# Performance work log

Measured on AMD Instinct MI355X. Metric: run time of the kernel, lower is better.

## Reference

```python
import jax, jax.numpy as jnp
import numpy as np

BLOCK = 64  # bitsandbytes 4-bit blocksize
OUT, IN = 4096, 4096
# NF4 codebook (bitsandbytes values)
NF4_CODE = np.array([
    -1.0, -0.6961928009986877, -0.5250730514526367, -0.39491748809814453,
    -0.28444138169288635, -0.18477343022823334, -0.09105003625154495, 0.0,
    0.07958029955625534, 0.16093020141124725, 0.24611230194568634,
    0.33791524171829224, 0.44070982933044434, 0.5626170039176941,
    0.7229568362236023, 1.0], dtype=np.float32)


def setup_inputs() -> dict:
    key = jax.random.key(0)
    k1, k2, k3 = jax.random.split(key, 3)
    x = jax.random.normal(k1, (8, 2048, IN), dtype=jnp.float32)
    qweight = jax.random.randint(k2, (OUT * IN,), 0, 16, dtype=jnp.int32)
    absmax = jax.random.uniform(k3, (OUT * IN // BLOCK,), dtype=jnp.float32)
    return {"x": x, "qweight": qweight, "absmax": absmax}


def reference(x, qweight, absmax):
    code = jnp.asarray(NF4_CODE)
    # dequantize: codebook lookup, then per-block absmax scaling
    w = code[qweight].reshape(-1, BLOCK) * absmax[:, None]  # [n_blocks, BLOCK]
    W = w.reshape(OUT, IN)                                   # [out, in]
    # linear: y = x @ W^T  (no bias: quantized_bias is None)
    return jnp.einsum('bsi,oi->bso', x, W)
```

## Files before the change

### kernel.cpp

```cpp
#include <hip/hip_runtime.h>
#include <hip/hip_bf16.h>
#include <stdint.h>

#define IN_DIM  4096
#define OUT_DIM 4096
#define M_DIM   16384
#define BK      64
#define NT      (IN_DIM / BK)

typedef float f32x4 __attribute__((ext_vector_type(4)));
typedef short bf16x8 __attribute__((ext_vector_type(8)));
typedef short bf16x4 __attribute__((ext_vector_type(4)));
typedef int   i32x4 __attribute__((ext_vector_type(4)));

__device__ __constant__ float NF4_CODE_D[16] = {
    -1.0f, -0.6961928009986877f, -0.5250730514526367f, -0.39491748809814453f,
    -0.28444138169288635f, -0.18477343022823334f, -0.09105003625154495f, 0.0f,
    0.07958029955625534f, 0.16093020141124725f, 0.24611230194568634f,
    0.33791524171829224f, 0.44070982933044434f, 0.5626170039176941f,
    0.7229568362236023f, 1.0f};

static __device__ __forceinline__ ushort f2bf(float f) {
  union { float f; uint32_t u; } v; v.f = f;
  uint32_t r = v.u + 0x7FFFu + ((v.u >> 16) & 1u);
  return (ushort)(r >> 16);
}

__global__ void dequant_nf4(const int* __restrict__ q, const float* __restrict__ am,
                            ushort* __restrict__ w) {
  __shared__ float code[16];
  if (threadIdx.x < 16) code[threadIdx.x] = NF4_CODE_D[threadIdx.x];
  __syncthreads();
  size_t t = (size_t)blockIdx.x * blockDim.x + threadIdx.x;
  size_t base = t * 8;
  i32x4 qa = *(const i32x4*)(q + base);
  i32x4 qb = *(const i32x4*)(q + base + 4);
  float s = am[base >> 6];
  bf16x8 o;
  o[0] = (short)f2bf(code[qa[0] & 15] * s);
  o[1] = (short)f2bf(code[qa[1] & 15] * s);
  o[2] = (short)f2bf(code[qa[2] & 15] * s);
  o[3] = (short)f2bf(code[qa[3] & 15] * s);
  o[4] = (short)f2bf(code[qb[0] & 15] * s);
  o[5] = (short)f2bf(code[qb[1] & 15] * s);
  o[6] = (short)f2bf(code[qb[2] & 15] * s);
  o[7] = (short)f2bf(code[qb[3] & 15] * s);
  *(bf16x8*)(w + base) = o;
}

__global__ void cvt_x(const float* __restrict__ x, ushort* __restrict__ xb) {
  size_t t = (size_t)blockIdx.x * blockDim.x + threadIdx.x;
  size_t base = t * 8;
  f32x4 a = *(const f32x4*)(x + base);
  f32x4 b = *(const f32x4*)(x + base + 4);
  bf16x8 o;
  o[0] = (short)f2bf(a[0]); o[1] = (short)f2bf(a[1]);
  o[2] = (short)f2bf(a[2]); o[3] = (short)f2bf(a[3]);
  o[4] = (short)f2bf(b[0]); o[5] = (short)f2bf(b[1]);
  o[6] = (short)f2bf(b[2]); o[7] = (short)f2bf(b[3]);
  *(bf16x8*)(xb + base) = o;
}

static __device__ __forceinline__ void llds16(const ushort* g, ushort* l) {
  __builtin_amdgcn_global_load_lds(
      (const __attribute__((address_space(1))) void*)g,
      (__attribute__((address_space(3))) void*)l, 16, 0, 0);
}

__global__ __launch_bounds__(512, 2) void gemm256(const ushort* __restrict__ Xb,
                                                  const ushort* __restrict__ W,
                                                  float* __restrict__ Y) {
  __shared__ ushort As[2][256 * BK];
  __shared__ ushort Bs[2][256 * BK];

  const int tid  = threadIdx.x;
  const int lane = tid & 63;
  const int wid  = tid >> 6;
  const int wr   = wid >> 2;
  const int wc   = wid & 3;
  const int l15  = lane & 15;
  const int kg   = lane >> 4;
  const int l7   = lane & 7;

  const int bid = blockIdx.x;
  const int wg  = (bid & 7) * 128 + (bid >> 3);
  const int tm  = wg >> 4;
  const int tn  = wg & 15;
  const size_t row0 = (size_t)tm * 256;
  const size_t col0 = (size_t)tn * 256;

  const int srow  = tid >> 3;
  const int scol8 = ((tid & 7) ^ (srow & 7)) * 8;
  const int wbase = wid << 9;

  f32x4  acc[8][4] = {};
  bf16x8 aA[4][2], aB[4][2], b0[2][2], b1[2][2];

#define BARX()  __builtin_amdgcn_s_barrier()
#define VMC(n)  asm volatile("s_waitcnt vmcnt(" #n ")" ::: "memory")
#define PRI1()  __builtin_amdgcn_s_setprio(1)
#define PRI0()  __builtin_amdgcn_s_setprio(0)

#define STAGE_A(kt, h, nb) do { \
    llds16(Xb + (row0 + (h)*128 +  0 + srow) * IN_DIM + (kt)*BK + scol8, \
           &As[nb][(h)*8192 +    0 + wbase]); \
    llds16(Xb + (row0 + (h)*128 + 64 + srow) * IN_DIM + (kt)*BK + scol8, \
           &As[nb][(h)*8192 + 4096 + wbase]); \
  } while (0)

#define STAGE_B(kt, h, nb) do { \
    llds16(W + (col0 + (h)*128 +  0 + srow) * IN_DIM + (kt)*BK + scol8, \
           &Bs[nb][(h)*8192 +    0 + wbase]); \
    llds16(W + (col0 + (h)*128 + 64 + srow) * IN_DIM + (kt)*BK + scol8, \
           &Bs[nb][(h)*8192 + 4096 + wbase]); \
  } while (0)

#define LDA_(dst, nb, mh) do { \
    _Pragma("unroll") for (int mi = 0; mi < 4; ++mi) \
    _Pragma("unroll") for (int ks = 0; ks < 2; ++ks) \
      dst[mi][ks] = *(const bf16x8*)&As[nb][((mh)*128 + wr*64 + mi*16 + l15) * BK \
                                            + (((ks*4 + kg) ^ l7) * 8)]; \
  } while (0)

#define LDB_(dst, nb, nh) do { \
    _Pragma("unroll") for (int ni = 0; ni < 2; ++ni) \
    _Pragma("unroll") for (int ks = 0; ks < 2; ++ks) \
      dst[ni][ks] = *(const bf16x8*)&Bs[nb][((nh)*128 + wc*32 + ni*16 + l15) * BK \
                                            + (((ks*4 + kg) ^ l7) * 8)]; \
  } while (0)

#define QUAD(mh, nh, aR, bR) do { PRI1(); \
    _Pragma("unroll") for (int mi = 0; mi < 4; ++mi) \
    _Pragma("unroll") for (int ni = 0; ni < 2; ++ni) \
    _Pragma("unroll") for (int ks = 0; ks < 2; ++ks) \
      acc[(mh)*4 + mi][(nh)*2 + ni] = __builtin_amdgcn_mfma_f32_16x16x32_bf16( \
          aR[mi][ks], bR[ni][ks], acc[(mh)*4 + mi][(nh)*2 + ni], 0, 0, 0); \
    PRI0(); } while (0)

  STAGE_A(0, 0, 0); STAGE_A(0, 1, 0);
  STAGE_B(0, 0, 0); STAGE_B(0, 1, 0);
  STAGE_A(1, 0, 1); STAGE_A(1, 1, 1);
  STAGE_B(1, 0, 1); STAGE_B(1, 1, 1);
  VMC(8); BARX();
  LDA_(aA, 0, 0); LDB_(b0, 0, 0);

#pragma unroll 1
  for (int t = 0; t < NT - 2; ++t) {
    const int cur = t & 1, nxt = cur ^ 1;
    LDB_(b1, cur, 1); LDA_(aB, cur, 1);
    QUAD(0, 0, aA, b0);
    BARX();
    STAGE_A(t + 2, 0, cur); STAGE_B(t + 2, 0, cur);
    QUAD(0, 1, aA, b1);
    BARX();
    QUAD(1, 1, aB, b1);
    BARX();
    STAGE_A(t + 2, 1, cur); STAGE_B(t + 2, 1, cur);
    VMC(8);
    BARX();
    QUAD(1, 0, aB, b0);
    LDA_(aA, nxt, 0); LDB_(b0, nxt, 0);
  }

  LDB_(b1, 0, 1); LDA_(aB, 0, 1);
  QUAD(0, 0, aA, b0);
  BARX();
  QUAD(0, 1, aA, b1);
  BARX();
  QUAD(1, 1, aB, b1);
  BARX();
  VMC(0);
  BARX();
  QUAD(1, 0, aB, b0);
  LDA_(aA, 1, 0); LDB_(b0, 1, 0);

  LDB_(b1, 1, 1); LDA_(aB, 1, 1);
  QUAD(0, 0, aA, b0);
  QUAD(0, 1, aA, b1);
  QUAD(1, 1, aB, b1);
  QUAD(1, 0, aB, b0);

#undef QUAD
#undef LDB_
#undef LDA_
#undef STAGE_B
#undef STAGE_A

  float* yb = Y + (row0 + wr * 64 + kg * 4) * OUT_DIM + col0 + wc * 32 + l15;
#pragma unroll
  for (int mh = 0; mh < 2; ++mh)
#pragma unroll
    for (int mi = 0; mi < 4; ++mi)
#pragma unroll
      for (int nh = 0; nh < 2; ++nh)
#pragma unroll
        for (int ni = 0; ni < 2; ++ni)
#pragma unroll
          for (int v = 0; v < 4; ++v)
            yb[(size_t)(mh * 128 + mi * 16 + v) * OUT_DIM + nh * 128 + ni * 16] =
                acc[mh * 4 + mi][nh * 2 + ni][v];
}

__global__ void gemm_fb(const float* __restrict__ X, const ushort* __restrict__ W,
                        float* __restrict__ Y) {
  __shared__ ushort Af[128 * 64];
  __shared__ ushort Bf[128 * 64];
  const int tid  = threadIdx.x;
  const int lane = tid & 63;
  const int wid  = tid >> 6;
  const int wr   = wid >> 1, wc = wid & 1;
  const int bid  = blockIdx.x;
  const int tm   = bid / 32, tn = bid % 32;
  const size_t row0 = (size_t)tm * 128, col0 = (size_t)tn * 128;
  f32x4 acc[4][4] = {};
  const int arow = lane & 15, kgrp = lane >> 4;
  const int srow = lane >> 3, scol = (lane & 7) * 8;
  for (int k0 = 0; k0 < IN_DIM; k0 += 64) {
    f32x4 r[8];
#pragma unroll
    for (int i = 0; i < 8; ++i)
      r[i] = *(const f32x4*)(X + (row0 + i * 16 + (tid >> 4)) * IN_DIM + k0 + (tid & 15) * 4);
#pragma unroll
    for (int i = 0; i < 8; ++i) {
      bf16x4 o;
      o[0] = (short)f2bf(r[i][0]); o[1] = (short)f2bf(r[i][1]);
      o[2] = (short)f2bf(r[i][2]); o[3] = (short)f2bf(r[i][3]);
      *(bf16x4*)&Af[(i * 16 + (tid >> 4)) * 64 + (tid & 15) * 4] = o;
    }
#pragma unroll
    for (int i = 0; i < 4; ++i) {
      const int c = wid * 4 + i;
      llds16(W + (col0 + c * 8 + srow) * IN_DIM + k0 + scol, Bf + c * 512);
    }
    __syncthreads();
#pragma unroll
    for (int ks = 0; ks < 2; ++ks) {
      bf16x8 a[4], b[4];
#pragma unroll
      for (int m = 0; m < 4; ++m)
        a[m] = *(const bf16x8*)&Af[(wr * 64 + m * 16 + arow) * 64 + ks * 32 + kgrp * 8];
#pragma unroll
      for (int n = 0; n < 4; ++n)
        b[n] = *(const bf16x8*)&Bf[(wc * 64 + n * 16 + arow) * 64 + ks * 32 + kgrp * 8];
#pragma unroll
      for (int m = 0; m < 4; ++m)
#pragma unroll
        for (int n = 0; n < 4; ++n)
          acc[m][n] = __builtin_amdgcn_mfma_f32_16x16x32_bf16(a[m], b[n], acc[m][n], 0, 0, 0);
    }
    __syncthreads();
  }
  float* yb = Y + (row0 + wr * 64) * OUT_DIM + col0 + wc * 64;
  const int crow = (lane >> 4) * 4, ccol = lane & 15;
#pragma unroll
  for (int m = 0; m < 4; ++m)
#pragma unroll
    for (int n = 0; n < 4; ++n)
#pragma unroll
      for (int v = 0; v < 4; ++v)
        yb[(size_t)(m * 16 + crow + v) * OUT_DIM + n * 16 + ccol] = acc[m][n][v];
}

extern "C" void kernel_launch(void* const* d_in, const int* in_sizes, int n_in,
                              void* d_out, int out_size, void* d_ws, size_t ws_size,
                              hipStream_t stream) {
  const float* x  = (const float*)d_in[0];
  const int*   q  = (const int*)d_in[1];
  const float* am = (const float*)d_in[2];
  float* y = (float*)d_out;

  ushort* w = (ushort*)d_ws;
  const size_t WB = (size_t)OUT_DIM * IN_DIM * sizeof(ushort);
  const size_t XB = (size_t)M_DIM * IN_DIM * sizeof(ushort);

  dequant_nf4<<<(OUT_DIM * (size_t)IN_DIM) / 8 / 256, 256, 0, stream>>>(q, am, w);

  if (ws_size >= WB + XB) {
    ushort* xb = (ushort*)((char*)d_ws + WB);
    cvt_x<<<((size_t)M_DIM * IN_DIM) / 8 / 256, 256, 0, stream>>>(x, xb);
    gemm256<<<(M_DIM / 256) * (OUT_DIM / 256), 512, 0, stream>>>(xb, w, y);
  } else {
    gemm_fb<<<(M_DIM / 128) * (OUT_DIM / 128), 256, 0, stream>>>(x, w, y);
  }
}
```

Before: 633.8 us.

## Reschedule GEMM main loop with interleaved LDS reads, stages, and explicit lgkmcnt waits

Restructures the double-buffered MFMA main loop so that each quadrant of MFMAs is paired with one LDS fragment load and one global-to-LDS stage. Explicit lgkmcnt and vmcnt waits plus sched_barrier replace the compiler's implicit waits, and the barrier becomes inline asm. The aim is to spread memory issue evenly between compute phases and keep the matrix cores fed. It adds barriers per iteration, and the hand-tuned wait counts risk hazards if the counts are wrong.

```diff
diff --git a/kernel.cpp b/kernel.cpp
--- a/kernel.cpp
+++ b/kernel.cpp
@@ -96,10 +96,13 @@
   f32x4  acc[8][4] = {};
   bf16x8 aA[4][2], aB[4][2], b0[2][2], b1[2][2];
 
-#define BARX()  __builtin_amdgcn_s_barrier()
-#define VMC(n)  asm volatile("s_waitcnt vmcnt(" #n ")" ::: "memory")
-#define PRI1()  __builtin_amdgcn_s_setprio(1)
-#define PRI0()  __builtin_amdgcn_s_setprio(0)
+#define BARX()   asm volatile("s_barrier" ::: "memory")
+#define LGKM0()  do { asm volatile("s_waitcnt lgkmcnt(0)" ::: "memory"); \
+                      __builtin_amdgcn_sched_barrier(0); } while (0)
+#define LGKM8()  asm volatile("s_waitcnt lgkmcnt(8)" ::: "memory")
+#define VMC(n)   asm volatile("s_waitcnt vmcnt(" #n ")" ::: "memory")
+#define PRI1()   __builtin_amdgcn_s_setprio(1)
+#define PRI0()   __builtin_amdgcn_s_setprio(0)
 
 #define STAGE_A(kt, h, nb) do { \
     llds16(Xb + (row0 + (h)*128 +  0 + srow) * IN_DIM + (kt)*BK + scol8, \
@@ -137,48 +140,61 @@
           aR[mi][ks], bR[ni][ks], acc[(mh)*4 + mi][(nh)*2 + ni], 0, 0, 0); \
     PRI0(); } while (0)
 
-  STAGE_A(0, 0, 0); STAGE_A(0, 1, 0);
-  STAGE_B(0, 0, 0); STAGE_B(0, 1, 0);
-  STAGE_A(1, 0, 1); STAGE_A(1, 1, 1);
-  STAGE_B(1, 0, 1); STAGE_B(1, 1, 1);
+  STAGE_A(0, 0, 0); STAGE_B(0, 0, 0); STAGE_A(0, 1, 0); STAGE_B(0, 1, 0);
+  STAGE_A(1, 0, 1); STAGE_B(1, 0, 1); STAGE_A(1, 1, 1); STAGE_B(1, 1, 1);
   VMC(8); BARX();
   LDA_(aA, 0, 0); LDB_(b0, 0, 0);
 
 #pragma unroll 1
   for (int t = 0; t < NT - 2; ++t) {
     const int cur = t & 1, nxt = cur ^ 1;
-    LDB_(b1, cur, 1); LDA_(aB, cur, 1);
+    LDA_(aB, cur, 1);
+    STAGE_A(t + 2, 0, cur);
+    BARX(); LGKM0();
     QUAD(0, 0, aA, b0);
     BARX();
-    STAGE_A(t + 2, 0, cur); STAGE_B(t + 2, 0, cur);
+    LDB_(b1, cur, 1);
+    STAGE_B(t + 2, 0, cur);
+    BARX(); LGKM0();
+    QUAD(1, 0, aB, b0);
+    BARX();
+    STAGE_A(t + 2, 1, cur);
+    VMC(10);
+    BARX(); LGKM0();
     QUAD(0, 1, aA, b1);
     BARX();
+    LDA_(aA, nxt, 0); LDB_(b0, nxt, 0);
+    STAGE_B(t + 2, 1, cur);
+    LGKM8();
+    VMC(8);
+    BARX(); LGKM0();
     QUAD(1, 1, aB, b1);
     BARX();
-    STAGE_A(t + 2, 1, cur); STAGE_B(t + 2, 1, cur);
-    VMC(8);
-    BARX();
-    QUAD(1, 0, aB, b0);
-    LDA_(aA, nxt, 0); LDB_(b0, nxt, 0);
   }
 
-  LDB_(b1, 0, 1); LDA_(aB, 0, 1);
+  LDA_(aB, 0, 1);
+  BARX(); LGKM0();
   QUAD(0, 0, aA, b0);
   BARX();
+  LDB_(b1, 0, 1);
+  BARX(); LGKM0();
+  QUAD(1, 0, aB, b0);
+  BARX();
+  VMC(4);
+  BARX(); LGKM0();
   QUAD(0, 1, aA, b1);
   BARX();
+  LDA_(aA, 1, 0); LDB_(b0, 1, 0);
+  LGKM8(); VMC(0);
+  BARX(); LGKM0();
   QUAD(1, 1, aB, b1);
   BARX();
-  VMC(0);
-  BARX();
+
+  LDA_(aB, 1, 1); LDB_(b1, 1, 1);
+  QUAD(0, 0, aA, b0);
   QUAD(1, 0, aB, b0);
-  LDA_(aA, 1, 0); LDB_(b0, 1, 0);
-
-  LDB_(b1, 1, 1); LDA_(aB, 1, 1);
-  QUAD(0, 0, aA, b0);
   QUAD(0, 1, aA, b1);
   QUAD(1, 1, aB, b1);
-  QUAD(1, 0, aB, b0);
 
 #undef QUAD
 #undef LDB_
```

Result: faster. 616.3 us (-2.8%).
